# Kernel optimization log

Measured on AMD Instinct MI355X. Metric: run time of the kernel, lower is better.

## Reference

```python
import jax, jax.numpy as jnp
import numpy as np

N_NODES = 100000
N_EDGES = 1600000
D_IN = 128
D_OUT = 128


def setup_inputs() -> dict:
    key = jax.random.key(0)
    k = jax.random.split(key, 7)
    x = jax.random.normal(k[0], (N_NODES, D_IN), dtype=jnp.float32)
    edge_index = jax.random.randint(k[1], (2, N_EDGES), 0, N_NODES, dtype=jnp.int32)
    # MLP params (PyTorch Linear-style scaling)
    s1 = 1.0 / np.sqrt(D_IN)
    s2 = 1.0 / np.sqrt(D_OUT)
    W1 = jax.random.uniform(k[2], (D_IN, D_OUT), jnp.float32, -s1, s1)
    b1 = jax.random.uniform(k[3], (D_OUT,), jnp.float32, -s1, s1)
    W2 = jax.random.uniform(k[4], (D_OUT, D_OUT), jnp.float32, -s2, s2)
    b2 = jax.random.uniform(k[5], (D_OUT,), jnp.float32, -s2, s2)
    eps = jnp.zeros((), dtype=jnp.float32)  # train_eps=True, init 0
    return {"x": x, "edge_index": edge_index, "W1": W1, "b1": b1, "W2": W2, "b2": b2, "eps": eps}


def reference(x, edge_index, W1, b1, W2, b2, eps):
    src, dst = edge_index[0], edge_index[1]  # flow: source_to_target
    # scatter-add neighbor aggregation: agg[i] = sum_{(j->i)} x[j]
    agg = jax.ops.segment_sum(x[src], dst, num_segments=x.shape[0])  # [N, D_IN]
    h = (1.0 + eps) * x + agg
    # 2-layer MLP: Linear -> ReLU -> Linear
    h = jax.nn.relu(h @ W1 + b1)
    return h @ W2 + b2
```

## Files before the change

### kernel.cpp

```cpp
#include <hip/hip_runtime.h>

#define NN    100000
#define NE    1600000
#define DD    128
#define CAP   48
#define NBKT  391
#define PCAP  4608
#define EPB   4096
#define NCVT  12500

typedef float  f4v __attribute__((ext_vector_type(4)));
typedef float  f2v __attribute__((ext_vector_type(2)));
typedef short  s8v __attribute__((ext_vector_type(8)));
typedef unsigned short u16;
typedef unsigned int   u32;

static __device__ __forceinline__ u16 f2bf(float f) {
    u32 u = __float_as_uint(f);
    return (u16)((u + 0x7fffu + ((u >> 16) & 1u)) >> 16);
}
static __device__ __forceinline__ f2v unpk(u32 p) {
    f2v r;
    r.x = __uint_as_float(p << 16);
    r.y = __uint_as_float(p & 0xffff0000u);
    return r;
}

static __device__ __forceinline__ void cvt_rows(
    const float* __restrict__ x, u32* __restrict__ xbp, int row_base, int tid)
{
    const int row  = row_base + (tid >> 6);
    const int lane = tid & 63;
    const float* xp = x + (size_t)row * DD;
    xbp[(size_t)row * 64 + lane] =
        (u32)f2bf(xp[lane]) | ((u32)f2bf(xp[lane + 64]) << 16);
}

__global__ __launch_bounds__(256) void part_conv(
    const float* __restrict__ x, const int* __restrict__ ei,
    u32* __restrict__ xbp, u32* __restrict__ pairs, int* __restrict__ gcnt)
{
    __shared__ int hist[NBKT];
    __shared__ int base[NBKT];
    const int b   = blockIdx.x;
    const int tid = threadIdx.x;
    if (b >= NBKT) {
        cvt_rows(x, xbp, (b - NBKT) * 4, tid);
        return;
    }
    const int e0 = b * EPB;

    int sv[16], dv[16];
#pragma unroll
    for (int t = 0; t < 16; ++t) {
        const int e = e0 + t * 256 + tid;
        if (e < NE) { sv[t] = ei[e]; dv[t] = ei[NE + e]; }
        else        { dv[t] = -1; sv[t] = 0; }
    }

    for (int i = tid; i < NBKT; i += 256) hist[i] = 0;
    __syncthreads();

#pragma unroll
    for (int t = 0; t < 16; ++t)
        if (dv[t] >= 0) atomicAdd(&hist[dv[t] >> 8], 1);
    __syncthreads();

    for (int i = tid; i < NBKT; i += 256) {
        const int h = hist[i];
        base[i] = h ? atomicAdd(&gcnt[i * 16], h) : 0;
        hist[i] = 0;
    }
    __syncthreads();

#pragma unroll
    for (int t = 0; t < 16; ++t)
        if (dv[t] >= 0) {
            const int bk = dv[t] >> 8;
            const int r  = base[bk] + atomicAdd(&hist[bk], 1);
            if (r < PCAP)
                pairs[(size_t)bk * PCAP + r] = ((u32)sv[t] << 8) | (u32)(dv[t] & 255);
        }
}

__global__ __launch_bounds__(256) void build_conv(
    const float* __restrict__ x,
    const float* __restrict__ W1, const float* __restrict__ W2,
    const u32* __restrict__ pairs, const int* __restrict__ gcnt,
    u32* __restrict__ xbp, u16* __restrict__ img1, u16* __restrict__ img2,
    int* __restrict__ cnt, int* __restrict__ eidx)
{
    __shared__ int cl[256], cur[256];
    const int b   = blockIdx.x;
    const int tid = threadIdx.x;

    if (b >= NBKT) {
        if (b < NBKT + NCVT) {
            cvt_rows(x, xbp, 50000 + (b - NBKT) * 4, tid);
        } else if (b < NBKT + NCVT + 8) {
            const int gid  = (b - NBKT - NCVT) * 256 + tid;
            const int frag = gid >> 6;
            const int lane = gid & 63;
            const int n  = (frag >> 2) * 16 + (lane & 15);
            const int k0 = (frag & 3) * 32 + (lane >> 4) * 8;
            u16* o1 = img1 + (size_t)gid * 8;
            u16* o2 = img2 + (size_t)gid * 8;
#pragma unroll
            for (int j = 0; j < 8; ++j) {
                o1[j] = f2bf(W1[(size_t)(k0 + j) * DD + n]);
                o2[j] = f2bf(W2[(size_t)(k0 + j) * DD + n]);
            }
        } else {
            if (tid < 64) xbp[(size_t)NN * 64 + tid] = 0;
        }
        return;
    }

    const int n   = min(gcnt[b * 16], PCAP);
    const u32* pp = pairs + (size_t)b * PCAP;

    u32 pv[18];
#pragma unroll
    for (int t = 0; t < 18; ++t) {
        const int i = t * 256 + tid;
        if (i < n) pv[t] = pp[i];
    }

    cl[tid] = 0; cur[tid] = 0;
    __syncthreads();

#pragma unroll
    for (int t = 0; t < 18; ++t) {
        const int i = t * 256 + tid;
        if (i < n) atomicAdd(&cl[pv[t] & 255], 1);
    }
    __syncthreads();

    const int g = b * 256 + tid;
    if (g < NN) cnt[g] = cl[tid];

#pragma unroll
    for (int t = 0; t < 18; ++t) {
        const int i = t * 256 + tid;
        if (i < n) {
            const u32 p  = pv[t];
            const int ld = p & 255;
            const int r  = atomicAdd(&cur[ld], 1);
            if (r < CAP) eidx[(size_t)(b * 256 + ld) * CAP + r] = (int)(p >> 8);
        }
    }
}

__global__ __launch_bounds__(256, 3) void gather_mlp(
    const u32* __restrict__ xbp, const int* __restrict__ cnt,
    const int* __restrict__ eidx, const float* __restrict__ epsp,
    const u16* __restrict__ img1, const u16* __restrict__ img2,
    const float* __restrict__ b1, const float* __restrict__ b2,
    float* __restrict__ out)
{
    __shared__ char rows[64 * 256];
    __shared__ char lds_raw[4 * 8448];

    const int tid  = threadIdx.x;
    const int wave = tid >> 6;
    const int lane = tid & 63;
    const int l15  = lane & 15;
    const int quad = lane >> 4;

    const int rb = blockIdx.x * 64 + wave * 16;

    const float sc = 1.0f + epsp[0];

    float bv1[8], bv2[8];
#pragma unroll
    for (int nt = 0; nt < 8; ++nt) {
        bv1[nt] = b1[nt * 16 + l15];
        bv2[nt] = b2[nt * 16 + l15];
    }

    int cv = 0;
    {
        int nd = rb + l15; if (nd > NN - 1) nd = NN - 1;
        if (lane < 16) cv = cnt[nd];
    }

    int idx[16];
#pragma unroll
    for (int n = 0; n < 16; ++n) {
        int nd = rb + n; if (nd > NN - 1) nd = NN - 1;
        const int dgc = min(__builtin_amdgcn_readlane(cv, n), CAP);
        const int v   = eidx[(size_t)nd * CAP + lane];
        idx[n] = (lane < dgc) ? v : NN;
    }

#pragma unroll
    for (int n = 0; n < 16; ++n) {
        int nd = rb + n; if (nd > NN - 1) nd = NN - 1;
        const int dgc = min(__builtin_amdgcn_readlane(cv, n), CAP);
        const u32 ps  = xbp[((size_t)nd << 6) + lane];
        const int nb  = (dgc + 15) >> 4;

        f2v a0 = {0.f, 0.f}, a1 = {0.f, 0.f}, a2 = {0.f, 0.f}, a3 = {0.f, 0.f};
        for (int bb = 0; bb < nb; ++bb) {
            u32 p[16];
#pragma unroll
            for (int t = 0; t < 16; ++t) {
                const u32 s = (u32)__builtin_amdgcn_readlane(idx[n], bb * 16 + t);
                p[t] = xbp[((size_t)s << 6) + lane];
            }
#pragma unroll
            for (int t = 0; t < 16; t += 4) {
                a0 += unpk(p[t]); a1 += unpk(p[t + 1]);
                a2 += unpk(p[t + 2]); a3 += unpk(p[t + 3]);
            }
        }
        const f2v st = (a0 + a1) + (a2 + a3);
        const f2v sv = unpk(ps);
        const u16 r0 = f2bf(fmaf(sc, sv.x, st.x));
        const u16 r1 = f2bf(fmaf(sc, sv.y, st.y));

        char* rp = rows + (wave * 16 + n) * 256;
        const int swz = (n & 7) << 4;
        *(u16*)(rp + ((lane * 2) ^ swz))       = r0;
        *(u16*)(rp + ((128 + lane * 2) ^ swz)) = r1;
    }
    __syncthreads();

    float* fstage = (float*)(lds_raw + wave * 8448);
    u16*   hstage = (u16*)fstage;

    s8v afrag[4];
#pragma unroll
    for (int kc = 0; kc < 4; ++kc) {
        const int boff = (kc * 64 + quad * 16) ^ ((l15 & 7) << 4);
        afrag[kc] = *(const s8v*)(rows + (wave * 16 + l15) * 256 + boff);
    }

    f4v acc1[8] = {};
#pragma unroll
    for (int kc = 0; kc < 4; ++kc)
#pragma unroll
        for (int nt = 0; nt < 8; ++nt) {
            const s8v bfr = *(const s8v*)(img1 + ((size_t)((nt * 4 + kc) * 64 + lane)) * 8);
            acc1[nt] = __builtin_amdgcn_mfma_f32_16x16x32_bf16(afrag[kc], bfr, acc1[nt], 0, 0, 0);
        }

#pragma unroll
    for (int nt = 0; nt < 8; ++nt)
#pragma unroll
        for (int r = 0; r < 4; ++r) {
            const float v = fmaxf(acc1[nt][r] + bv1[nt], 0.0f);
            hstage[(quad * 4 + r) * 136 + nt * 16 + l15] = f2bf(v);
        }
    __syncthreads();

    s8v a2f[4];
#pragma unroll
    for (int kc = 0; kc < 4; ++kc)
        a2f[kc] = *(const s8v*)&hstage[l15 * 136 + kc * 32 + quad * 8];

    f4v acc2[8] = {};
#pragma unroll
    for (int kc = 0; kc < 4; ++kc)
#pragma unroll
        for (int nt = 0; nt < 8; ++nt) {
            const s8v bfr = *(const s8v*)(img2 + ((size_t)((nt * 4 + kc) * 64 + lane)) * 8);
            acc2[nt] = __builtin_amdgcn_mfma_f32_16x16x32_bf16(a2f[kc], bfr, acc2[nt], 0, 0, 0);
        }

    __syncthreads();
#pragma unroll
    for (int nt = 0; nt < 8; ++nt)
#pragma unroll
        for (int r = 0; r < 4; ++r)
            fstage[(quad * 4 + r) * 132 + nt * 16 + l15] = acc2[nt][r] + bv2[nt];
    __syncthreads();

#pragma unroll
    for (int i = 0; i < 8; ++i) {
        const int m  = (lane >> 5) + 2 * i;
        const int c4 = lane & 31;
        if (rb + m < NN) {
            const f4v v = *(const f4v*)&fstage[m * 132 + c4 * 4];
            *(f4v*)(out + (size_t)(rb + m) * DD + c4 * 4) = v;
        }
    }
}

extern "C" void kernel_launch(void* const* d_in, const int* in_sizes, int n_in,
                              void* d_out, int out_size, void* d_ws, size_t ws_size,
                              hipStream_t stream) {
    const float* x   = (const float*)d_in[0];
    const int*   ei  = (const int*)d_in[1];
    const float* W1  = (const float*)d_in[2];
    const float* b1  = (const float*)d_in[3];
    const float* W2  = (const float*)d_in[4];
    const float* b2  = (const float*)d_in[5];
    const float* eps = (const float*)d_in[6];
    float* out = (float*)d_out;

    u32* xbp   = (u32*)d_ws;
    int* eidx  = (int*)(xbp + (size_t)(NN + 1) * 64);
    int* cnt   = eidx + (size_t)NN * CAP + 64;
    u16* img1  = (u16*)(cnt + NN);
    u16* img2  = img1 + (size_t)DD * DD;
    u32* pairs = (u32*)(img2 + (size_t)DD * DD);
    int* gcnt  = (int*)(pairs + (size_t)NBKT * PCAP);

    hipMemsetAsync(gcnt, 0, (size_t)NBKT * 16 * sizeof(int), stream);
    part_conv <<<NBKT + NCVT,     256, 0, stream>>>(x, ei, xbp, pairs, gcnt);
    build_conv<<<NBKT + NCVT + 9, 256, 0, stream>>>(x, W1, W2, pairs, gcnt,
                                                    xbp, img1, img2, cnt, eidx);
    gather_mlp<<<(NN + 63) / 64,  256, 0, stream>>>(xbp, cnt, eidx, eps,
                                                    img1, img2, b1, b2, out);
}
```

Baseline: 234.4 us.

## Shrink gather_mlp LDS to per-wave buffer, drop block barriers, raise occupancy

Each wave now stages its 16 aggregated rows and the hidden activations in one private 4 KB LDS region, with a swizzled layout, instead of a shared rows buffer plus a separate staging buffer. All __syncthreads calls are removed because each wave touches only its own LDS. The output is written straight from the MFMA accumulators to global memory rather than through an LDS transpose, and launch bounds rise from 3 to 7 blocks to allow more resident waves. The cost is narrower 4-byte scattered global stores in place of 16-byte row stores, and more register pressure under the tighter launch bound.

```diff
diff --git a/kernel.cpp b/kernel.cpp
--- a/kernel.cpp
+++ b/kernel.cpp
@@ -151,15 +151,14 @@
     }
 }
 
-__global__ __launch_bounds__(256, 3) void gather_mlp(
+__global__ __launch_bounds__(256, 7) void gather_mlp(
     const u32* __restrict__ xbp, const int* __restrict__ cnt,
     const int* __restrict__ eidx, const float* __restrict__ epsp,
     const u16* __restrict__ img1, const u16* __restrict__ img2,
     const float* __restrict__ b1, const float* __restrict__ b2,
     float* __restrict__ out)
 {
-    __shared__ char rows[64 * 256];
-    __shared__ char lds_raw[4 * 8448];
+    __shared__ char rows[4 * 4096];
 
     const int tid  = threadIdx.x;
     const int wave = tid >> 6;
@@ -167,6 +166,7 @@
     const int l15  = lane & 15;
     const int quad = lane >> 4;
 
+    char* wbase = rows + wave * 4096;
     const int rb = blockIdx.x * 64 + wave * 16;
 
     const float sc = 1.0f + epsp[0];
@@ -219,21 +219,17 @@
         const u16 r0 = f2bf(fmaf(sc, sv.x, st.x));
         const u16 r1 = f2bf(fmaf(sc, sv.y, st.y));
 
-        char* rp = rows + (wave * 16 + n) * 256;
+        char* rp = wbase + n * 256;
         const int swz = (n & 7) << 4;
         *(u16*)(rp + ((lane * 2) ^ swz))       = r0;
         *(u16*)(rp + ((128 + lane * 2) ^ swz)) = r1;
     }
-    __syncthreads();
-
-    float* fstage = (float*)(lds_raw + wave * 8448);
-    u16*   hstage = (u16*)fstage;
 
     s8v afrag[4];
 #pragma unroll
     for (int kc = 0; kc < 4; ++kc) {
         const int boff = (kc * 64 + quad * 16) ^ ((l15 & 7) << 4);
-        afrag[kc] = *(const s8v*)(rows + (wave * 16 + l15) * 256 + boff);
+        afrag[kc] = *(const s8v*)(wbase + l15 * 256 + boff);
     }
 
     f4v acc1[8] = {};
@@ -249,15 +245,18 @@
     for (int nt = 0; nt < 8; ++nt)
 #pragma unroll
         for (int r = 0; r < 4; ++r) {
+            const int hr = quad * 4 + r;
             const float v = fmaxf(acc1[nt][r] + bv1[nt], 0.0f);
-            hstage[(quad * 4 + r) * 136 + nt * 16 + l15] = f2bf(v);
-        }
-    __syncthreads();
+            const int boff = hr * 256 + (((nt * 16 + l15) * 2) ^ ((hr & 7) << 4));
+            *(u16*)(wbase + boff) = f2bf(v);
+        }
 
     s8v a2f[4];
 #pragma unroll
-    for (int kc = 0; kc < 4; ++kc)
-        a2f[kc] = *(const s8v*)&hstage[l15 * 136 + kc * 32 + quad * 8];
+    for (int kc = 0; kc < 4; ++kc) {
+        const int boff = (kc * 64 + quad * 16) ^ ((l15 & 7) << 4);
+        a2f[kc] = *(const s8v*)(wbase + l15 * 256 + boff);
+    }
 
     f4v acc2[8] = {};
 #pragma unroll
@@ -268,23 +267,14 @@
             acc2[nt] = __builtin_amdgcn_mfma_f32_16x16x32_bf16(a2f[kc], bfr, acc2[nt], 0, 0, 0);
         }
 
-    __syncthreads();
 #pragma unroll
     for (int nt = 0; nt < 8; ++nt)
 #pragma unroll
-        for (int r = 0; r < 4; ++r)
-            fstage[(quad * 4 + r) * 132 + nt * 16 + l15] = acc2[nt][r] + bv2[nt];
-    __syncthreads();
-
-#pragma unroll
-    for (int i = 0; i < 8; ++i) {
-        const int m  = (lane >> 5) + 2 * i;
-        const int c4 = lane & 31;
-        if (rb + m < NN) {
-            const f4v v = *(const f4v*)&fstage[m * 132 + c4 * 4];
-            *(f4v*)(out + (size_t)(rb + m) * DD + c4 * 4) = v;
-        }
-    }
+        for (int r = 0; r < 4; ++r) {
+            const int m = quad * 4 + r;
+            if (rb + m < NN)
+                out[(size_t)(rb + m) * DD + nt * 16 + l15] = acc2[nt][r] + bv2[nt];
+        }
 }
 
 extern "C" void kernel_launch(void* const* d_in, const int* in_sizes, int n_in,
```

Measured after the change: 249.2 us. 6.3% more time.
